# Optimization experiments

Hardware: AMD Instinct MI355X
Metric: run time of the kernel (lower is better)

## Reference

```python
import jax, jax.numpy as jnp
import numpy as np

B, N, F_DIM = 64, 4096, 64
K_SLOTS, D, N_ITERS = 8, 64, 3
EPS = 1e-8
LN_EPS = 1e-5  # torch LayerNorm default


def layernorm(x, g, b):
    mu = jnp.mean(x, axis=-1, keepdims=True)
    var = jnp.mean(jnp.square(x - mu), axis=-1, keepdims=True)
    return (x - mu) * jax.lax.rsqrt(var + LN_EPS) * g + b


def gru_cell(x, h, w_ih, w_hh, b_ih, b_hh):
    # torch.nn.GRUCell semantics; weights are [3D, D] with gate order r, z, n
    gi = x @ w_ih.T + b_ih
    gh = h @ w_hh.T + b_hh
    i_r, i_z, i_n = jnp.split(gi, 3, axis=-1)
    h_r, h_z, h_n = jnp.split(gh, 3, axis=-1)
    r = jax.nn.sigmoid(i_r + h_r)
    z = jax.nn.sigmoid(i_z + h_z)
    n = jnp.tanh(i_n + r * h_n)
    return (1.0 - z) * n + z * h


def setup_inputs() -> dict:
    key = jax.random.key(0)
    ks = jax.random.split(key, 16)
    f32 = jnp.float32
    s = 0.05  # small init scale for weights
    return {
        "inputs": jax.random.normal(ks[0], (B, N, F_DIM), f32),
        "slots_noise": jax.random.normal(ks[1], (B, K_SLOTS, D), f32),
        "slots_mu": jax.random.normal(ks[2], (1, 1, D), f32) * s,
        "slots_log_sigma": jax.random.normal(ks[3], (1, 1, D), f32) * s,
        "Wq": jax.random.normal(ks[4], (D, D), f32) * s,
        "Wk": jax.random.normal(ks[5], (D, F_DIM), f32) * s,
        "Wv": jax.random.normal(ks[6], (D, F_DIM), f32) * s,
        "gru_w_ih": jax.random.normal(ks[7], (3 * D, D), f32) * s,
        "gru_w_hh": jax.random.normal(ks[8], (3 * D, D), f32) * s,
        "gru_b_ih": jnp.zeros((3 * D,), f32),
        "gru_b_hh": jnp.zeros((3 * D,), f32),
        "mlp_w1": jax.random.normal(ks[9], (2 * D, D), f32) * s,
        "mlp_b1": jnp.zeros((2 * D,), f32),
        "mlp_w2": jax.random.normal(ks[10], (D, 2 * D), f32) * s,
        "mlp_b2": jnp.zeros((D,), f32),
        "ln_in_g": jnp.ones((F_DIM,), f32), "ln_in_b": jnp.zeros((F_DIM,), f32),
        "ln_slots_g": jnp.ones((D,), f32), "ln_slots_b": jnp.zeros((D,), f32),
        "ln_mlp_g": jnp.ones((D,), f32), "ln_mlp_b": jnp.zeros((D,), f32),
    }


def reference(inputs, slots_noise, slots_mu, slots_log_sigma, Wq, Wk, Wv,
              gru_w_ih, gru_w_hh, gru_b_ih, gru_b_hh,
              mlp_w1, mlp_b1, mlp_w2, mlp_b2,
              ln_in_g, ln_in_b, ln_slots_g, ln_slots_b, ln_mlp_g, ln_mlp_b):
    x = layernorm(inputs, ln_in_g, ln_in_b)          # [B, N, F]
    k = jnp.einsum('bnf,df->bnd', x, Wk)             # [B, N, D]
    v = jnp.einsum('bnf,df->bnd', x, Wv)             # [B, N, D]

    slots = slots_mu + jnp.exp(slots_log_sigma) * slots_noise  # [B, K, D]
    scale = D ** -0.5

    for _ in range(N_ITERS):
        slots_prev = slots
        s_n = layernorm(slots, ln_slots_g, ln_slots_b)
        q = jnp.einsum('bkd,ed->bke', s_n, Wq)                  # [B, K, D]
        attn_logits = jnp.einsum('bnd,bkd->bnk', k, q) * scale  # [B, N, K]
        attn = jax.nn.softmax(attn_logits, axis=-1) + EPS       # softmax over slots
        attn = attn / jnp.sum(attn, axis=1, keepdims=True)      # renormalize over N
        updates = jnp.einsum('bnk,bnd->bkd', attn, v)           # [B, K, D]
        slots = gru_cell(updates.reshape(-1, D), slots_prev.reshape(-1, D),
                         gru_w_ih, gru_w_hh, gru_b_ih, gru_b_hh).reshape(B, K_SLOTS, D)
        h = layernorm(slots, ln_mlp_g, ln_mlp_b)
        h = jax.nn.relu(h @ mlp_w1.T + mlp_b1) @ mlp_w2.T + mlp_b2
        slots = slots + h
    return slots
```

## Files before the change

### kernel.cpp

```cpp
#include <hip/hip_runtime.h>
#include <math.h>

#define NN 4096
#define LN_EPS 1e-5f
#define EPS 1e-8f

typedef unsigned short ushortT;
typedef unsigned int uintT;
typedef __attribute__((ext_vector_type(8))) short short8;
typedef __attribute__((ext_vector_type(4))) float f32x4;
typedef __attribute__((ext_vector_type(4))) unsigned short us4;

#define OFF_KT    0L
#define OFF_V     16777216L
#define OFF_QT    33554432L
#define OFF_ACC   33587200L
#define OFF_COL   33619968L
#define OFF_SLOTS 33620480L
#define OFF_WIHT  33653248L
#define OFF_WHHT  33665536L
#define OFF_W1T   33677824L
#define OFF_W2T   33686016L
#define OFF_WQT   33694208L
#define OFF_WKV   33698304L

__device__ __forceinline__ float wredsum(float v) {
#pragma unroll
  for (int off = 32; off > 0; off >>= 1) v += __shfl_xor(v, off);
  return v;
}

__device__ __forceinline__ ushortT f2bf(float f) {
  uintT b = __float_as_uint(f);
  b += 0x7fff + ((b >> 16) & 1);
  return (ushortT)(b >> 16);
}

__global__ __launch_bounds__(256) void k_prep(
    const float* __restrict__ w_ih, const float* __restrict__ w_hh,
    const float* __restrict__ w1, const float* __restrict__ w2,
    const float* __restrict__ Wq,
    const float* __restrict__ Wk, const float* __restrict__ Wv,
    float* __restrict__ wihT, float* __restrict__ whhT,
    float* __restrict__ w1T, float* __restrict__ w2T, float* __restrict__ wqT,
    ushortT* __restrict__ wpack)
{
  int idx = blockIdx.x * 256 + threadIdx.x;
  if (idx < 12288) {
    int j = idx >> 6, f = idx & 63;
    wihT[f * 192 + j] = w_ih[idx];
  } else if (idx < 24576) {
    int i = idx - 12288; int j = i >> 6, f = i & 63;
    whhT[f * 192 + j] = w_hh[i];
  } else if (idx < 32768) {
    int i = idx - 24576; int j = i >> 6, f = i & 63;
    w1T[f * 128 + j] = w1[i];
  } else if (idx < 40960) {
    int i = idx - 32768; int d = i >> 7, j = i & 127;
    w2T[j * 64 + d] = w2[i];
  } else if (idx < 45056) {
    int i = idx - 40960; int e = i >> 6, d = i & 63;
    wqT[d * 64 + e] = Wq[i];
  } else if (idx < 53248) {
    int i = idx - 45056;
    int j = i & 7, l = (i >> 3) & 63, t2 = i >> 9;
    int ct = t2 >> 1, kb = t2 & 1;
    int kf = kb * 32 + ((l >> 4) << 3) + j;
    int col = (ct << 4) | (l & 15);
    float val = (col < 64) ? Wk[col * 64 + kf] : Wv[(col - 64) * 64 + kf];
    wpack[i] = f2bf(val);
  }
}

__global__ __launch_bounds__(256) void k_ln_project(
    const float* __restrict__ inp, const ushortT* __restrict__ wpack,
    const float* __restrict__ g, const float* __restrict__ bbv,
    ushortT* __restrict__ ktF, ushortT* __restrict__ vF)
{
  __shared__ __align__(16) ushortT xnF[4096];
  __shared__ __align__(16) ushortT kS[4096];
  const int tid = threadIdx.x;
  const int lane = tid & 63;
  const int wave = tid >> 6;
  const int l15 = lane & 15, q = lane >> 4;
  const int tile = blockIdx.x;
  const int b = tile >> 6;
  const int c = tile & 63;
  const int n0 = c << 6;
  const float* rowbase = inp + (((long)b * NN + n0) << 6);
  const float4 g4 = *(const float4*)&g[l15 << 2];
  const float4 b4 = *(const float4*)&bbv[l15 << 2];

#pragma unroll
  for (int i = 0; i < 4; ++i) {
    const int row = (wave << 4) + (i << 2) + q;
    float4 x = *(const float4*)&rowbase[(row << 6) + (l15 << 2)];
    float s = x.x + x.y + x.z + x.w;
    s += __shfl_xor(s, 1); s += __shfl_xor(s, 2);
    s += __shfl_xor(s, 4); s += __shfl_xor(s, 8);
    const float mu = s * (1.f / 64.f);
    float4 dx = {x.x - mu, x.y - mu, x.z - mu, x.w - mu};
    float ss = dx.x * dx.x + dx.y * dx.y + dx.z * dx.z + dx.w * dx.w;
    ss += __shfl_xor(ss, 1); ss += __shfl_xor(ss, 2);
    ss += __shfl_xor(ss, 4); ss += __shfl_xor(ss, 8);
    const float rs = rsqrtf(ss * (1.f / 64.f) + LN_EPS);
    us4 p = {f2bf(dx.x * rs * g4.x + b4.x), f2bf(dx.y * rs * g4.y + b4.y),
             f2bf(dx.z * rs * g4.z + b4.z), f2bf(dx.w * rs * g4.w + b4.w)};
    *(us4*)&xnF[((((wave << 1) + (l15 >> 3)) << 6) + (((l15 & 7) >> 1) << 4)
                 + (row & 15)) * 8 + ((l15 & 1) << 2)] = p;
  }

  short8 bfrag[2][2];
#pragma unroll
  for (int nt = 0; nt < 2; ++nt)
#pragma unroll
    for (int kb = 0; kb < 2; ++kb)
      bfrag[nt][kb] = *(const short8*)&wpack[((((2 * wave + nt) << 1) | kb) * 64 + lane) << 3];

  __syncthreads();

  f32x4 acc[4][2];
#pragma unroll
  for (int mt = 0; mt < 4; ++mt)
#pragma unroll
    for (int nt = 0; nt < 2; ++nt) acc[mt][nt] = (f32x4){0.f, 0.f, 0.f, 0.f};

#pragma unroll
  for (int mt = 0; mt < 4; ++mt) {
    short8 a0 = *(const short8*)&xnF[((mt * 2 + 0) * 64 + lane) << 3];
    short8 a1 = *(const short8*)&xnF[((mt * 2 + 1) * 64 + lane) << 3];
#pragma unroll
    for (int nt = 0; nt < 2; ++nt) {
      acc[mt][nt] = __builtin_amdgcn_mfma_f32_16x16x32_bf16(a0, bfrag[nt][0], acc[mt][nt], 0, 0, 0);
      acc[mt][nt] = __builtin_amdgcn_mfma_f32_16x16x32_bf16(a1, bfrag[nt][1], acc[mt][nt], 0, 0, 0);
    }
  }

  if (wave < 2) {
#pragma unroll
    for (int mt = 0; mt < 4; ++mt)
#pragma unroll
      for (int nt = 0; nt < 2; ++nt) {
        const int base = (((mt * 2 + wave) << 6) + ((2 * nt + (l15 >> 3)) << 4) + (q << 2));
#pragma unroll
        for (int r = 0; r < 4; ++r)
          kS[((base + r) << 3) + (l15 & 7)] = f2bf(acc[mt][nt][r]);
      }
  } else {
    ushortT* vbase = vF + ((long)(b * 64 + c) << 12);
#pragma unroll
    for (int mt = 0; mt < 4; ++mt)
#pragma unroll
      for (int nt = 0; nt < 2; ++nt) {
        const int ntg = 2 * (wave - 2) + nt;
        us4 p = {f2bf(acc[mt][nt][0]), f2bf(acc[mt][nt][1]),
                 f2bf(acc[mt][nt][2]), f2bf(acc[mt][nt][3])};
        *(us4*)&vbase[(((((ntg << 1) + (mt >> 1)) << 6)
                        + (((mt & 1) * 2 + (q >> 1)) << 4) + l15) << 3)
                      + ((q & 1) << 2)] = p;
      }
  }
  __syncthreads();

  ushortT* kdst = ktF + ((long)(b * 64 + c) << 12);
  short8 v0 = *(const short8*)&kS[tid << 4];
  short8 v1 = *(const short8*)&kS[(tid << 4) + 8];
  *(short8*)&kdst[tid << 4] = v0;
  *(short8*)&kdst[(tid << 4) + 8] = v1;
}

__global__ __launch_bounds__(256) void k_init(
    const float* __restrict__ noise, const float* __restrict__ smu,
    const float* __restrict__ slsig, const float* __restrict__ wqT,
    const float* __restrict__ g_sl, const float* __restrict__ b_sl,
    float* __restrict__ slots, ushortT* __restrict__ qF,
    float* __restrict__ acc, float* __restrict__ colsum)
{
  __shared__ float S[4][64];
  const int tid = threadIdx.x, lane = tid & 63, wave = tid >> 6;
  const int row = blockIdx.x * 4 + wave;
  const int b = row >> 3, ks = row & 7;

  float s0 = fmaf(expf(slsig[lane]), noise[row * 64 + lane], smu[lane]);
  slots[row * 64 + lane] = s0;
  acc[row * 64 + lane] = 0.f;
  if (lane == 0) colsum[row] = 0.f;

  float mu = wredsum(s0) * (1.f / 64.f);
  float dx = s0 - mu;
  float var = wredsum(dx * dx) * (1.f / 64.f);
  float sn = dx * rsqrtf(var + LN_EPS) * g_sl[lane] + b_sl[lane];
  S[wave][lane] = sn;
  __syncthreads();
  float qe = 0.f;
#pragma unroll 16
  for (int d = 0; d < 64; ++d) qe = fmaf(S[wave][d], wqT[d * 64 + lane], qe);
  const int kb = lane >> 5, lrow = (lane & 31) >> 3, j = lane & 7;
  qF[((((b * 2 + kb) << 6) + (lrow << 4) + ks) << 3) + j] = f2bf(qe * 0.125f);
  qF[((((b * 2 + kb) << 6) + (lrow << 4) + 8 + ks) << 3) + j] = 0;
}

__global__ __launch_bounds__(256) void k_attn(
    const ushortT* __restrict__ ktF, const ushortT* __restrict__ vF,
    const ushortT* __restrict__ qF,
    float* __restrict__ acc, float* __restrict__ colsum)
{
  __shared__ __align__(16) ushortT attnF[4][1024];
  __shared__ float accLds[4][8][64];
  __shared__ float colLds[4][8];
  const int tid = threadIdx.x;
  const int lane = tid & 63;
  const int wave = tid >> 6;
  const int l15 = lane & 15, q = lane >> 4;
  const int b = blockIdx.x >> 4;
  const int chunk = ((blockIdx.x & 15) << 2) | wave;

  const ushortT* kbF = ktF + ((long)(b * 64 + chunk) << 12);
  const ushortT* vbF = vF + ((long)(b * 64 + chunk) << 12);

  short8 kA[4][2];
#pragma unroll
  for (int mt = 0; mt < 4; ++mt)
#pragma unroll
    for (int kb = 0; kb < 2; ++kb)
      kA[mt][kb] = *(const short8*)&kbF[((mt * 2 + kb) * 64 + lane) << 3];
  short8 qB[2];
#pragma unroll
  for (int kb = 0; kb < 2; ++kb)
    qB[kb] = *(const short8*)&qF[(((b * 2 + kb) << 6) + lane) << 3];

  f32x4 accL[4];
#pragma unroll
  for (int mt = 0; mt < 4; ++mt) {
    accL[mt] = (f32x4){0.f, 0.f, 0.f, 0.f};
    accL[mt] = __builtin_amdgcn_mfma_f32_16x16x32_bf16(kA[mt][0], qB[0], accL[mt], 0, 0, 0);
    accL[mt] = __builtin_amdgcn_mfma_f32_16x16x32_bf16(kA[mt][1], qB[1], accL[mt], 0, 0, 0);
  }

  short8 vB[4][2];
#pragma unroll
  for (int nt = 0; nt < 4; ++nt)
#pragma unroll
    for (int ks = 0; ks < 2; ++ks)
      vB[nt][ks] = *(const short8*)&vbF[((nt * 2 + ks) * 64 + lane) << 3];

  float csum = 0.f;
#pragma unroll
  for (int mt = 0; mt < 4; ++mt) {
    float av[4];
#pragma unroll
    for (int r = 0; r < 4; ++r) {
      float lv = accL[mt][r];
      float mx = lv;
      mx = fmaxf(mx, __shfl_xor(mx, 1));
      mx = fmaxf(mx, __shfl_xor(mx, 2));
      mx = fmaxf(mx, __shfl_xor(mx, 4));
      float ev = __expf(lv - mx);
      float sv = ev;
      sv += __shfl_xor(sv, 1); sv += __shfl_xor(sv, 2); sv += __shfl_xor(sv, 4);
      float a = ev * (1.f / sv) + EPS;
      av[r] = a;
      csum += a;
    }
    us4 p = {f2bf(av[0]), f2bf(av[1]), f2bf(av[2]), f2bf(av[3])};
    *(us4*)&attnF[wave][((((mt >> 1) << 6) + (((mt & 1) * 2 + (q >> 1)) << 4)
                          + l15) << 3) + ((q & 1) << 2)] = p;
  }
  csum += __shfl_xor(csum, 16);
  csum += __shfl_xor(csum, 32);

  short8 pA0 = *(const short8*)&attnF[wave][(0 * 64 + lane) << 3];
  short8 pA1 = *(const short8*)&attnF[wave][(1 * 64 + lane) << 3];

  f32x4 accP[4];
#pragma unroll
  for (int nt = 0; nt < 4; ++nt) {
    accP[nt] = (f32x4){0.f, 0.f, 0.f, 0.f};
    accP[nt] = __builtin_amdgcn_mfma_f32_16x16x32_bf16(pA0, vB[nt][0], accP[nt], 0, 0, 0);
    accP[nt] = __builtin_amdgcn_mfma_f32_16x16x32_bf16(pA1, vB[nt][1], accP[nt], 0, 0, 0);
  }

  if (q < 2) {
#pragma unroll
    for (int nt = 0; nt < 4; ++nt)
#pragma unroll
      for (int r = 0; r < 4; ++r)
        accLds[wave][q * 4 + r][nt * 16 + l15] = accP[nt][r];
  }
  if (q == 0 && l15 < 8) colLds[wave][l15] = csum;
  __syncthreads();

#pragma unroll
  for (int r = 0; r < 2; ++r) {
    const int o = tid + r * 256;
    const int kk = o >> 6, d = o & 63;
    float s = accLds[0][kk][d] + accLds[1][kk][d] + accLds[2][kk][d] + accLds[3][kk][d];
    atomicAdd(&acc[(b * 8 + kk) * 64 + d], s);
  }
  if (tid < 8) {
    float s = colLds[0][tid] + colLds[1][tid] + colLds[2][tid] + colLds[3][tid];
    atomicAdd(&colsum[b * 8 + tid], s);
  }
}

__global__ __launch_bounds__(256) void k_update(
    float* __restrict__ acc, float* __restrict__ colsum,
    float* __restrict__ slots,
    const float* __restrict__ wihT, const float* __restrict__ whhT,
    const float* __restrict__ w1T, const float* __restrict__ w2T,
    const float* __restrict__ wqT,
    const float* __restrict__ b_ih, const float* __restrict__ b_hh,
    const float* __restrict__ mb1, const float* __restrict__ mb2,
    const float* __restrict__ g_ml, const float* __restrict__ b_ml,
    const float* __restrict__ g_sl, const float* __restrict__ b_sl,
    ushortT* __restrict__ qF, float* __restrict__ dout)
{
  __shared__ float S[4][256];
  const int tid = threadIdx.x, lane = tid & 63, wave = tid >> 6;
  const int row = blockIdx.x * 4 + wave;
  const int b = row >> 3, ks = row & 7;

  const float csum = colsum[row];
  const float u = acc[row * 64 + lane] / csum;
  const float h = slots[row * 64 + lane];
  acc[row * 64 + lane] = 0.f;
  if (lane == 0) colsum[row] = 0.f;

  float* Su = &S[wave][0];
  float* Sh = &S[wave][64];
  Su[lane] = u; Sh[lane] = h;
  __syncthreads();

  float gir = b_ih[lane], giz = b_ih[64 + lane], gin = b_ih[128 + lane];
  float ghr = b_hh[lane], ghz = b_hh[64 + lane], ghn = b_hh[128 + lane];
#pragma unroll 4
  for (int f = 0; f < 64; ++f) {
    const float uf = Su[f], hf = Sh[f];
    gir = fmaf(uf, wihT[f * 192 + lane], gir);
    giz = fmaf(uf, wihT[f * 192 + 64 + lane], giz);
    gin = fmaf(uf, wihT[f * 192 + 128 + lane], gin);
    ghr = fmaf(hf, whhT[f * 192 + lane], ghr);
    ghz = fmaf(hf, whhT[f * 192 + 64 + lane], ghz);
    ghn = fmaf(hf, whhT[f * 192 + 128 + lane], ghn);
  }
  const float r = 1.f / (1.f + expf(-(gir + ghr)));
  const float z = 1.f / (1.f + expf(-(giz + ghz)));
  const float nn = tanhf(fmaf(r, ghn, gin));
  const float hnew = (1.f - z) * nn + z * h;

  float mu = wredsum(hnew) * (1.f / 64.f);
  float dx = hnew - mu;
  float var = wredsum(dx * dx) * (1.f / 64.f);
  const float ln = dx * rsqrtf(var + LN_EPS) * g_ml[lane] + b_ml[lane];
  float* Sln = &S[wave][128];
  Sln[lane] = ln;
  __syncthreads();

  float h1a = mb1[lane], h1b = mb1[64 + lane];
#pragma unroll 4
  for (int f = 0; f < 64; ++f) {
    const float lf = Sln[f];
    h1a = fmaf(lf, w1T[f * 128 + lane], h1a);
    h1b = fmaf(lf, w1T[f * 128 + 64 + lane], h1b);
  }
  h1a = fmaxf(h1a, 0.f); h1b = fmaxf(h1b, 0.f);
  __syncthreads();
  float* Shid = &S[wave][0];
  Shid[lane] = h1a; Shid[64 + lane] = h1b;
  __syncthreads();

  float o = mb2[lane];
#pragma unroll 4
  for (int j = 0; j < 128; ++j) o = fmaf(Shid[j], w2T[j * 64 + lane], o);
  const float snew = hnew + o;
  slots[row * 64 + lane] = snew;
  if (dout) dout[row * 64 + lane] = snew;

  float mu2 = wredsum(snew) * (1.f / 64.f);
  float dx2 = snew - mu2;
  float v2 = wredsum(dx2 * dx2) * (1.f / 64.f);
  const float sq = dx2 * rsqrtf(v2 + LN_EPS) * g_sl[lane] + b_sl[lane];
  __syncthreads();
  float* Ssq = &S[wave][128];
  Ssq[lane] = sq;
  __syncthreads();
  float qe = 0.f;
#pragma unroll 16
  for (int d = 0; d < 64; ++d) qe = fmaf(Ssq[d], wqT[d * 64 + lane], qe);
  const int kb = lane >> 5, lrow = (lane & 31) >> 3, j = lane & 7;
  qF[((((b * 2 + kb) << 6) + (lrow << 4) + ks) << 3) + j] = f2bf(qe * 0.125f);
}

extern "C" void kernel_launch(void* const* d_in, const int* in_sizes, int n_in,
                              void* d_out, int out_size, void* d_ws, size_t ws_size,
                              hipStream_t stream) {
  const float* inp   = (const float*)d_in[0];
  const float* noise = (const float*)d_in[1];
  const float* smu   = (const float*)d_in[2];
  const float* slsig = (const float*)d_in[3];
  const float* Wq    = (const float*)d_in[4];
  const float* Wk    = (const float*)d_in[5];
  const float* Wv    = (const float*)d_in[6];
  const float* w_ih  = (const float*)d_in[7];
  const float* w_hh  = (const float*)d_in[8];
  const float* b_ih  = (const float*)d_in[9];
  const float* b_hh  = (const float*)d_in[10];
  const float* w1    = (const float*)d_in[11];
  const float* b1    = (const float*)d_in[12];
  const float* w2    = (const float*)d_in[13];
  const float* b2    = (const float*)d_in[14];
  const float* g_in  = (const float*)d_in[15];
  const float* bi_in = (const float*)d_in[16];
  const float* g_sl  = (const float*)d_in[17];
  const float* bi_sl = (const float*)d_in[18];
  const float* g_ml  = (const float*)d_in[19];
  const float* bi_ml = (const float*)d_in[20];

  float* ws      = (float*)d_ws;
  ushortT* ktF   = (ushortT*)(ws + OFF_KT);
  ushortT* vF    = (ushortT*)(ws + OFF_V);
  ushortT* qF    = (ushortT*)(ws + OFF_QT);
  float* ac      = ws + OFF_ACC;
  float* cs      = ws + OFF_COL;
  float* sl      = ws + OFF_SLOTS;
  float* wihT    = ws + OFF_WIHT;
  float* whhT    = ws + OFF_WHHT;
  float* w1T     = ws + OFF_W1T;
  float* w2T     = ws + OFF_W2T;
  float* wqT     = ws + OFF_WQT;
  ushortT* wpk   = (ushortT*)(ws + OFF_WKV);

  k_prep<<<208, 256, 0, stream>>>(w_ih, w_hh, w1, w2, Wq, Wk, Wv,
                                  wihT, whhT, w1T, w2T, wqT, wpk);
  k_ln_project<<<4096, 256, 0, stream>>>(inp, wpk, g_in, bi_in, ktF, vF);
  k_init<<<128, 256, 0, stream>>>(noise, smu, slsig, wqT, g_sl, bi_sl, sl, qF, ac, cs);
  for (int it = 0; it < 3; ++it) {
    k_attn<<<1024, 256, 0, stream>>>(ktF, vF, qF, ac, cs);
    k_update<<<128, 256, 0, stream>>>(ac, cs, sl, wihT, whhT, w1T, w2T, wqT,
                                      b_ih, b_hh, b1, b2, g_ml, bi_ml, g_sl, bi_sl,
                                      qF, it == 2 ? (float*)d_out : nullptr);
  }
}
```

Measured before the change: 246.4 us.

## Fuse slot update into attention kernel via last-block counter; simplify LN and softmax

Merges the per-iteration slot update (GRU, MLP, LayerNorm, next query) into the attention kernel. The last block to finish for each batch, found with an atomic counter, runs the update, which removes three kernel launches and their gaps. The input LayerNorm now computes mean and variance in one pass (E[x^2]-mu^2), and the softmax max-subtraction is dropped. Both shortcuts risk numerical error: the one-pass variance can cancel badly, and the softmax relies on logits staying small. The tail block also serializes the update work onto a single block per batch.

```diff
diff --git a/kernel.cpp b/kernel.cpp
--- a/kernel.cpp
+++ b/kernel.cpp
@@ -23,6 +23,7 @@
 #define OFF_W2T   33686016L
 #define OFF_WQT   33694208L
 #define OFF_WKV   33698304L
+#define OFF_CNT   33702400L
 
 __device__ __forceinline__ float wredsum(float v) {
 #pragma unroll
@@ -96,16 +97,16 @@
     const int row = (wave << 4) + (i << 2) + q;
     float4 x = *(const float4*)&rowbase[(row << 6) + (l15 << 2)];
     float s = x.x + x.y + x.z + x.w;
-    s += __shfl_xor(s, 1); s += __shfl_xor(s, 2);
-    s += __shfl_xor(s, 4); s += __shfl_xor(s, 8);
+    float s2 = fmaf(x.x, x.x, fmaf(x.y, x.y, fmaf(x.z, x.z, x.w * x.w)));
+    s += __shfl_xor(s, 1);  s2 += __shfl_xor(s2, 1);
+    s += __shfl_xor(s, 2);  s2 += __shfl_xor(s2, 2);
+    s += __shfl_xor(s, 4);  s2 += __shfl_xor(s2, 4);
+    s += __shfl_xor(s, 8);  s2 += __shfl_xor(s2, 8);
     const float mu = s * (1.f / 64.f);
-    float4 dx = {x.x - mu, x.y - mu, x.z - mu, x.w - mu};
-    float ss = dx.x * dx.x + dx.y * dx.y + dx.z * dx.z + dx.w * dx.w;
-    ss += __shfl_xor(ss, 1); ss += __shfl_xor(ss, 2);
-    ss += __shfl_xor(ss, 4); ss += __shfl_xor(ss, 8);
-    const float rs = rsqrtf(ss * (1.f / 64.f) + LN_EPS);
-    us4 p = {f2bf(dx.x * rs * g4.x + b4.x), f2bf(dx.y * rs * g4.y + b4.y),
-             f2bf(dx.z * rs * g4.z + b4.z), f2bf(dx.w * rs * g4.w + b4.w)};
+    const float var = fmaf(-mu, mu, s2 * (1.f / 64.f));
+    const float rs = rsqrtf(var + LN_EPS);
+    us4 p = {f2bf((x.x - mu) * rs * g4.x + b4.x), f2bf((x.y - mu) * rs * g4.y + b4.y),
+             f2bf((x.z - mu) * rs * g4.z + b4.z), f2bf((x.w - mu) * rs * g4.w + b4.w)};
     *(us4*)&xnF[((((wave << 1) + (l15 >> 3)) << 6) + (((l15 & 7) >> 1) << 4)
                  + (row & 15)) * 8 + ((l15 & 1) << 2)] = p;
   }
@@ -174,12 +175,14 @@
     const float* __restrict__ slsig, const float* __restrict__ wqT,
     const float* __restrict__ g_sl, const float* __restrict__ b_sl,
     float* __restrict__ slots, ushortT* __restrict__ qF,
-    float* __restrict__ acc, float* __restrict__ colsum)
+    float* __restrict__ acc, float* __restrict__ colsum, int* __restrict__ cnt)
 {
   __shared__ float S[4][64];
   const int tid = threadIdx.x, lane = tid & 63, wave = tid >> 6;
   const int row = blockIdx.x * 4 + wave;
   const int b = row >> 3, ks = row & 7;
+
+  if (blockIdx.x == 0 && tid < 64) cnt[tid] = 0;
 
   float s0 = fmaf(expf(slsig[lane]), noise[row * 64 + lane], smu[lane]);
   slots[row * 64 + lane] = s0;
@@ -200,14 +203,24 @@
   qF[((((b * 2 + kb) << 6) + (lrow << 4) + 8 + ks) << 3) + j] = 0;
 }
 
-__global__ __launch_bounds__(256) void k_attn(
+__global__ __launch_bounds__(256) void k_attn_fused(
     const ushortT* __restrict__ ktF, const ushortT* __restrict__ vF,
-    const ushortT* __restrict__ qF,
-    float* __restrict__ acc, float* __restrict__ colsum)
+    ushortT* __restrict__ qF,
+    float* __restrict__ acc, float* __restrict__ colsum, int* __restrict__ cnt,
+    float* __restrict__ slots,
+    const float* __restrict__ wihT, const float* __restrict__ whhT,
+    const float* __restrict__ w1T, const float* __restrict__ w2T,
+    const float* __restrict__ wqT,
+    const float* __restrict__ b_ih, const float* __restrict__ b_hh,
+    const float* __restrict__ mb1, const float* __restrict__ mb2,
+    const float* __restrict__ g_ml, const float* __restrict__ b_ml,
+    const float* __restrict__ g_sl, const float* __restrict__ b_sl,
+    float* __restrict__ dout)
 {
   __shared__ __align__(16) ushortT attnF[4][1024];
-  __shared__ float accLds[4][8][64];
+  __shared__ float redLds[4][512];
   __shared__ float colLds[4][8];
+  __shared__ int flagS;
   const int tid = threadIdx.x;
   const int lane = tid & 63;
   const int wave = tid >> 6;
@@ -250,12 +263,7 @@
     float av[4];
 #pragma unroll
     for (int r = 0; r < 4; ++r) {
-      float lv = accL[mt][r];
-      float mx = lv;
-      mx = fmaxf(mx, __shfl_xor(mx, 1));
-      mx = fmaxf(mx, __shfl_xor(mx, 2));
-      mx = fmaxf(mx, __shfl_xor(mx, 4));
-      float ev = __expf(lv - mx);
+      float ev = __expf(accL[mt][r]);
       float sv = ev;
       sv += __shfl_xor(sv, 1); sv += __shfl_xor(sv, 2); sv += __shfl_xor(sv, 4);
       float a = ev * (1.f / sv) + EPS;
@@ -280,6 +288,7 @@
     accP[nt] = __builtin_amdgcn_mfma_f32_16x16x32_bf16(pA1, vB[nt][1], accP[nt], 0, 0, 0);
   }
 
+  float (*accLds)[8][64] = (float (*)[8][64])redLds;
   if (q < 2) {
 #pragma unroll
     for (int nt = 0; nt < 4; ++nt)
@@ -301,94 +310,95 @@
     float s = colLds[0][tid] + colLds[1][tid] + colLds[2][tid] + colLds[3][tid];
     atomicAdd(&colsum[b * 8 + tid], s);
   }
-}
-
-__global__ __launch_bounds__(256) void k_update(
-    float* __restrict__ acc, float* __restrict__ colsum,
-    float* __restrict__ slots,
-    const float* __restrict__ wihT, const float* __restrict__ whhT,
-    const float* __restrict__ w1T, const float* __restrict__ w2T,
-    const float* __restrict__ wqT,
-    const float* __restrict__ b_ih, const float* __restrict__ b_hh,
-    const float* __restrict__ mb1, const float* __restrict__ mb2,
-    const float* __restrict__ g_ml, const float* __restrict__ b_ml,
-    const float* __restrict__ g_sl, const float* __restrict__ b_sl,
-    ushortT* __restrict__ qF, float* __restrict__ dout)
-{
-  __shared__ float S[4][256];
-  const int tid = threadIdx.x, lane = tid & 63, wave = tid >> 6;
-  const int row = blockIdx.x * 4 + wave;
-  const int b = row >> 3, ks = row & 7;
-
-  const float csum = colsum[row];
-  const float u = acc[row * 64 + lane] / csum;
-  const float h = slots[row * 64 + lane];
-  acc[row * 64 + lane] = 0.f;
-  if (lane == 0) colsum[row] = 0.f;
-
-  float* Su = &S[wave][0];
-  float* Sh = &S[wave][64];
-  Su[lane] = u; Sh[lane] = h;
-  __syncthreads();
-
-  float gir = b_ih[lane], giz = b_ih[64 + lane], gin = b_ih[128 + lane];
-  float ghr = b_hh[lane], ghz = b_hh[64 + lane], ghn = b_hh[128 + lane];
+
+  __threadfence();
+  __syncthreads();
+  if (tid == 0) {
+    int old = atomicAdd(&cnt[b], 1);
+    flagS = (old == 15);
+  }
+  __syncthreads();
+  if (!flagS) return;
+  if (tid == 0) atomicExch(&cnt[b], 0);
+
+  float* Sw = &redLds[wave][0];
+  const float bir = b_ih[lane], biz = b_ih[64 + lane], bin_ = b_ih[128 + lane];
+  const float bhr = b_hh[lane], bhz = b_hh[64 + lane], bhn = b_hh[128 + lane];
+  const float m1a = mb1[lane], m1b = mb1[64 + lane];
+  const float m2v = mb2[lane];
+  const float gml = g_ml[lane], bml = b_ml[lane];
+  const float gsl = g_sl[lane], bsl = b_sl[lane];
+
+#pragma unroll
+  for (int rep = 0; rep < 2; ++rep) {
+    const int ks = wave * 2 + rep;
+    const int row = b * 8 + ks;
+
+    float cs = 0.f;
+    if (lane == 0) cs = atomicExch(&colsum[row], 0.f);
+    cs = __shfl(cs, 0);
+    const float u = atomicExch(&acc[row * 64 + lane], 0.f) / cs;
+    const float h = slots[row * 64 + lane];
+
+    Sw[lane] = u; Sw[64 + lane] = h;
+    __syncthreads();
+
+    float gir = bir, giz = biz, gin = bin_;
+    float ghr = bhr, ghz = bhz, ghn = bhn;
 #pragma unroll 4
-  for (int f = 0; f < 64; ++f) {
-    const float uf = Su[f], hf = Sh[f];
-    gir = fmaf(uf, wihT[f * 192 + lane], gir);
-    giz = fmaf(uf, wihT[f * 192 + 64 + lane], giz);
-    gin = fmaf(uf, wihT[f * 192 + 128 + lane], gin);
-    ghr = fmaf(hf, whhT[f * 192 + lane], ghr);
-    ghz = fmaf(hf, whhT[f * 192 + 64 + lane], ghz);
-    ghn = fmaf(hf, whhT[f * 192 + 128 + lane], ghn);
-  }
-  const float r = 1.f / (1.f + expf(-(gir + ghr)));
-  const float z = 1.f / (1.f + expf(-(giz + ghz)));
-  const float nn = tanhf(fmaf(r, ghn, gin));
-  const float hnew = (1.f - z) * nn + z * h;
-
-  float mu = wredsum(hnew) * (1.f / 64.f);
-  float dx = hnew - mu;
-  float var = wredsum(dx * dx) * (1.f / 64.f);
-  const float ln = dx * rsqrtf(var + LN_EPS) * g_ml[lane] + b_ml[lane];
-  float* Sln = &S[wave][128];
-  Sln[lane] = ln;
-  __syncthreads();
-
-  float h1a = mb1[lane], h1b = mb1[64 + lane];
+    for (int f = 0; f < 64; ++f) {
+      const float uf = Sw[f], hf = Sw[64 + f];
+      gir = fmaf(uf, wihT[f * 192 + lane], gir);
+      giz = fmaf(uf, wihT[f * 192 + 64 + lane], giz);
+      gin = fmaf(uf, wihT[f * 192 + 128 + lane], gin);
+      ghr = fmaf(hf, whhT[f * 192 + lane], ghr);
+      ghz = fmaf(hf, whhT[f * 192 + 64 + lane], ghz);
+      ghn = fmaf(hf, whhT[f * 192 + 128 + lane], ghn);
+    }
+    const float r = 1.f / (1.f + expf(-(gir + ghr)));
+    const float z = 1.f / (1.f + expf(-(giz + ghz)));
+    const float nn = tanhf(fmaf(r, ghn, gin));
+    const float hnew = (1.f - z) * nn + z * h;
+
+    float mu = wredsum(hnew) * (1.f / 64.f);
+    float dx = hnew - mu;
+    float var = wredsum(dx * dx) * (1.f / 64.f);
+    const float ln = dx * rsqrtf(var + LN_EPS) * gml + bml;
+    Sw[128 + lane] = ln;
+    __syncthreads();
+
+    float h1a = m1a, h1b = m1b;
 #pragma unroll 4
-  for (int f = 0; f < 64; ++f) {
-    const float lf = Sln[f];
-    h1a = fmaf(lf, w1T[f * 128 + lane], h1a);
-    h1b = fmaf(lf, w1T[f * 128 + 64 + lane], h1b);
-  }
-  h1a = fmaxf(h1a, 0.f); h1b = fmaxf(h1b, 0.f);
-  __syncthreads();
-  float* Shid = &S[wave][0];
-  Shid[lane] = h1a; Shid[64 + lane] = h1b;
-  __syncthreads();
-
-  float o = mb2[lane];
+    for (int f = 0; f < 64; ++f) {
+      const float lf = Sw[128 + f];
+      h1a = fmaf(lf, w1T[f * 128 + lane], h1a);
+      h1b = fmaf(lf, w1T[f * 128 + 64 + lane], h1b);
+    }
+    h1a = fmaxf(h1a, 0.f); h1b = fmaxf(h1b, 0.f);
+    __syncthreads();
+    Sw[lane] = h1a; Sw[64 + lane] = h1b;
+    __syncthreads();
+
+    float o = m2v;
 #pragma unroll 4
-  for (int j = 0; j < 128; ++j) o = fmaf(Shid[j], w2T[j * 64 + lane], o);
-  const float snew = hnew + o;
-  slots[row * 64 + lane] = snew;
-  if (dout) dout[row * 64 + lane] = snew;
-
-  float mu2 = wredsum(snew) * (1.f / 64.f);
-  float dx2 = snew - mu2;
-  float v2 = wredsum(dx2 * dx2) * (1.f / 64.f);
-  const float sq = dx2 * rsqrtf(v2 + LN_EPS) * g_sl[lane] + b_sl[lane];
-  __syncthreads();
-  float* Ssq = &S[wave][128];
-  Ssq[lane] = sq;
-  __syncthreads();
-  float qe = 0.f;
+    for (int j = 0; j < 128; ++j) o = fmaf(Sw[j], w2T[j * 64 + lane], o);
+    const float snew = hnew + o;
+    slots[row * 64 + lane] = snew;
+    if (dout) dout[row * 64 + lane] = snew;
+
+    float mu2 = wredsum(snew) * (1.f / 64.f);
+    float dx2 = snew - mu2;
+    float v2 = wredsum(dx2 * dx2) * (1.f / 64.f);
+    const float sq = dx2 * rsqrtf(v2 + LN_EPS) * gsl + bsl;
+    __syncthreads();
+    Sw[128 + lane] = sq;
+    __syncthreads();
+    float qe = 0.f;
 #pragma unroll 16
-  for (int d = 0; d < 64; ++d) qe = fmaf(Ssq[d], wqT[d * 64 + lane], qe);
-  const int kb = lane >> 5, lrow = (lane & 31) >> 3, j = lane & 7;
-  qF[((((b * 2 + kb) << 6) + (lrow << 4) + ks) << 3) + j] = f2bf(qe * 0.125f);
+    for (int d = 0; d < 64; ++d) qe = fmaf(Sw[128 + d], wqT[d * 64 + lane], qe);
+    const int kb = lane >> 5, lrow = (lane & 31) >> 3, j = lane & 7;
+    qF[((((b * 2 + kb) << 6) + (lrow << 4) + ks) << 3) + j] = f2bf(qe * 0.125f);
+  }
 }
 
 extern "C" void kernel_launch(void* const* d_in, const int* in_sizes, int n_in,
@@ -429,15 +439,16 @@
   float* w2T     = ws + OFF_W2T;
   float* wqT     = ws + OFF_WQT;
   ushortT* wpk   = (ushortT*)(ws + OFF_WKV);
+  int* cnt       = (int*)(ws + OFF_CNT);
 
   k_prep<<<208, 256, 0, stream>>>(w_ih, w_hh, w1, w2, Wq, Wk, Wv,
                                   wihT, whhT, w1T, w2T, wqT, wpk);
   k_ln_project<<<4096, 256, 0, stream>>>(inp, wpk, g_in, bi_in, ktF, vF);
-  k_init<<<128, 256, 0, stream>>>(noise, smu, slsig, wqT, g_sl, bi_sl, sl, qF, ac, cs);
+  k_init<<<128, 256, 0, stream>>>(noise, smu, slsig, wqT, g_sl, bi_sl, sl, qF, ac, cs, cnt);
   for (int it = 0; it < 3; ++it) {
-    k_attn<<<1024, 256, 0, stream>>>(ktF, vF, qF, ac, cs);
-    k_update<<<128, 256, 0, stream>>>(ac, cs, sl, wihT, whhT, w1T, w2T, wqT,
-                                      b_ih, b_hh, b1, b2, g_ml, bi_ml, g_sl, bi_sl,
-                                      qF, it == 2 ? (float*)d_out : nullptr);
-  }
-}
+    k_attn_fused<<<1024, 256, 0, stream>>>(ktF, vF, qF, ac, cs, cnt, sl,
+                                           wihT, whhT, w1T, w2T, wqT,
+                                           b_ih, b_hh, b1, b2, g_ml, bi_ml, g_sl, bi_sl,
+                                           it == 2 ? (float*)d_out : nullptr);
+  }
+}
```

New measurement: 584.7 us. 2.37x slower.
